# Kernel tuning notes

Measured on AMD Instinct MI355X. Metric: run time of the kernel, lower is better.

Reference implementation:

```python
import jax, jax.numpy as jnp
import numpy as np

L, S, N, E, H = 1024, 2048, 4, 512, 8
HD = E // H
LN_EPS = 1e-5


def embed_rotary(x, cos, sin):
    # x, cos, sin: (N, T, E). Rotates interleaved even/odd feature pairs.
    x2 = jnp.stack([-x[..., 1::2], x[..., ::2]], axis=-1).reshape(x.shape)
    return x * cos + x2 * sin


def setup_inputs() -> dict:
    key = jax.random.key(0)
    ks = jax.random.split(key, 8)
    query = jax.random.normal(ks[0], (L, N, E), jnp.float32)
    value = jax.random.normal(ks[1], (S, N, E), jnp.float32)
    # rotary PE tables: [..., 0] = cos, [..., 1] = sin of per-position angles
    qa = jax.random.uniform(ks[2], (N, L, E), jnp.float32, 0.0, 2.0 * np.pi)
    ka = jax.random.uniform(ks[3], (N, S, E), jnp.float32, 0.0, 2.0 * np.pi)
    query_pos = jnp.stack([jnp.cos(qa), jnp.sin(qa)], axis=-1)
    value_pos = jnp.stack([jnp.cos(ka), jnp.sin(ka)], axis=-1)
    w_scale = 1.0 / np.sqrt(E)
    in_proj_weight = jax.random.normal(ks[4], (3 * E, E), jnp.float32) * w_scale
    in_proj_bias = jnp.zeros((3 * E,), jnp.float32)
    out_proj_weight = jax.random.normal(ks[5], (E, E), jnp.float32) * w_scale
    out_proj_bias = jnp.zeros((E,), jnp.float32)
    ln_gamma = jnp.ones((E,), jnp.float32)
    ln_beta = jnp.zeros((E,), jnp.float32)
    return {
        'query': query, 'value': value,
        'query_pos': query_pos, 'value_pos': value_pos,
        'in_proj_weight': in_proj_weight, 'in_proj_bias': in_proj_bias,
        'out_proj_weight': out_proj_weight, 'out_proj_bias': out_proj_bias,
        'ln_gamma': ln_gamma, 'ln_beta': ln_beta,
    }


def reference(query, value, query_pos, value_pos,
              in_proj_weight, in_proj_bias,
              out_proj_weight, out_proj_bias,
              ln_gamma, ln_beta):
    Lq, Nb, Em = query.shape
    scaling = (Em // H) ** -0.5
    # kv_same path of the custom MHA: q from W[:E], (k, v) from W[E:] chunked
    q = query @ in_proj_weight[:Em].T + in_proj_bias[:Em]
    kv = value @ in_proj_weight[Em:].T + in_proj_bias[Em:]
    k, v = kv[..., :Em], kv[..., Em:]
    q = q * scaling
    # rotary PE (applied batch-first, then back to (L, N, E))
    q = embed_rotary(q.transpose(1, 0, 2), query_pos[..., 0], query_pos[..., 1]).transpose(1, 0, 2)
    k = embed_rotary(k.transpose(1, 0, 2), value_pos[..., 0], value_pos[..., 1]).transpose(1, 0, 2)
    # (L, N, E) -> (N, H, L, HD), matching torch view(L, N*H, HD).transpose(0, 1)
    qh = q.reshape(Lq, Nb, H, HD).transpose(1, 2, 0, 3)
    kh = k.reshape(-1, Nb, H, HD).transpose(1, 2, 0, 3)
    vh = v.reshape(-1, Nb, H, HD).transpose(1, 2, 0, 3)
    attn = jax.nn.softmax(jnp.einsum('nhld,nhsd->nhls', qh, kh), axis=-1)
    out = jnp.einsum('nhls,nhsd->nhld', attn, vh)  # (N, H, L, HD)
    out = out.transpose(2, 0, 1, 3).reshape(Lq, Nb, Em)
    out = out @ out_proj_weight.T + out_proj_bias
    # residual + LayerNorm
    y = query + out
    mu = jnp.mean(y, axis=-1, keepdims=True)
    var = jnp.mean(jnp.square(y - mu), axis=-1, keepdims=True)
    y = (y - mu) / jnp.sqrt(var + LN_EPS) * ln_gamma + ln_beta
    return y
```

## Files before the change

kernel.cpp:

```cpp
#include <hip/hip_runtime.h>
#include <math.h>

#define L_  1024
#define S_  2048
#define NB  4
#define E_  512
#define H_  8
#define HD_ 64
#define SPLIT 2

constexpr float SCALING = 0.125f;
constexpr float LOG2E   = 1.44269504f;
constexpr float LNEPS   = 1e-5f;

typedef __attribute__((ext_vector_type(8))) short s16x8;
typedef __attribute__((ext_vector_type(8))) unsigned short u16x8;
typedef __attribute__((ext_vector_type(4))) float f32x4;
typedef unsigned short ushort_t;

__device__ __forceinline__ unsigned short f2bf(float f) {
    unsigned u = __builtin_bit_cast(unsigned, f);
    u += 0x7fffu + ((u >> 16) & 1u);
    return (unsigned short)(u >> 16);
}
__device__ __forceinline__ float bf2f(unsigned short h) {
    unsigned u = ((unsigned)h) << 16;
    return __builtin_bit_cast(float, u);
}
__device__ __forceinline__ unsigned packbf(float a, float b) {
    return (unsigned)f2bf(a) | ((unsigned)f2bf(b) << 16);
}

__global__ __launch_bounds__(256)
void cast4_kernel(const float* __restrict__ s0, const float* __restrict__ s1,
                  const float* __restrict__ s2, const float* __restrict__ s3,
                  ushort_t* __restrict__ d0, ushort_t* __restrict__ d1,
                  ushort_t* __restrict__ d2, ushort_t* __restrict__ d3,
                  int c0, int c1, int c2, int c3)
{
    int i = blockIdx.x * 256 + threadIdx.x;
    const float* s; ushort_t* d; int off;
    if      (i < c0) { s = s0; d = d0; off = i; }
    else if (i < c1) { s = s1; d = d1; off = i - c0; }
    else if (i < c2) { s = s2; d = d2; off = i - c1; }
    else if (i < c3) { s = s3; d = d3; off = i - c2; }
    else return;
    const float4* sp = (const float4*)(s + (size_t)off * 8);
    float4 a = sp[0], b = sp[1];
    u16x8 o;
    o[0] = f2bf(a.x); o[1] = f2bf(a.y); o[2] = f2bf(a.z); o[3] = f2bf(a.w);
    o[4] = f2bf(b.x); o[5] = f2bf(b.y); o[6] = f2bf(b.z); o[7] = f2bf(b.w);
    *(u16x8*)(d + (size_t)off * 8) = o;
}

__global__ __launch_bounds__(256)
void qkv_gemm_kernel(const ushort_t* __restrict__ qbf,
                     const ushort_t* __restrict__ vbf,
                     const ushort_t* __restrict__ wbf,
                     ushort_t* __restrict__ qC,
                     ushort_t* __restrict__ kvC)
{
    __shared__ ushort_t As[128 * 32];
    __shared__ ushort_t Bs[128 * 32];
    const int t = threadIdx.x;
    const int w = t >> 6, l = t & 63;
    const int wr = w >> 1, wc = w & 1;
    const int g = l >> 4, c16 = l & 15;

    const int bid = blockIdx.x;
    const ushort_t *A, *W;
    ushort_t* C;
    int nfeat, m0, n0;
    if (bid < 128) {
        A = qbf; W = wbf; C = qC; nfeat = 512;
        n0 = (bid & 3) * 128; m0 = (bid >> 2) * 128;
    } else {
        int b = bid - 128;
        A = vbf; W = wbf + 512 * 512; C = kvC; nfeat = 1024;
        n0 = (b & 7) * 128; m0 = (b >> 3) * 128;
    }

    f32x4 acc[4][4];
    #pragma unroll
    for (int m = 0; m < 4; ++m)
        #pragma unroll
        for (int n = 0; n < 4; ++n) acc[m][n] = (f32x4){0.f, 0.f, 0.f, 0.f};

    for (int k0 = 0; k0 < 512; k0 += 32) {
        #pragma unroll
        for (int ch = t; ch < 512; ch += 256) {
            int r = ch >> 2, c = ch & 3;
            s16x8 v = *(const s16x8*)(A + (size_t)(m0 + r) * 512 + k0 + c * 8);
            int cp = c ^ ((r >> 1) & 3);
            *(s16x8*)((char*)As + r * 64 + cp * 16) = v;
        }
        #pragma unroll
        for (int ch = t; ch < 512; ch += 256) {
            int r = ch >> 2, c = ch & 3;
            s16x8 v = *(const s16x8*)(W + (size_t)(n0 + r) * 512 + k0 + c * 8);
            int cp = c ^ ((r >> 1) & 3);
            *(s16x8*)((char*)Bs + r * 64 + cp * 16) = v;
        }
        __syncthreads();
        s16x8 fa[4], fb[4];
        #pragma unroll
        for (int m = 0; m < 4; ++m) {
            int r = wr * 64 + m * 16 + c16;
            fa[m] = *(const s16x8*)((char*)As + r * 64 + ((g ^ ((r >> 1) & 3)) * 16));
        }
        #pragma unroll
        for (int n = 0; n < 4; ++n) {
            int r = wc * 64 + n * 16 + c16;
            fb[n] = *(const s16x8*)((char*)Bs + r * 64 + ((g ^ ((r >> 1) & 3)) * 16));
        }
        #pragma unroll
        for (int m = 0; m < 4; ++m)
            #pragma unroll
            for (int n = 0; n < 4; ++n)
                acc[m][n] = __builtin_amdgcn_mfma_f32_16x16x32_bf16(fa[m], fb[n], acc[m][n], 0, 0, 0);
        __syncthreads();
    }

    #pragma unroll
    for (int m = 0; m < 4; ++m) {
        #pragma unroll
        for (int n = 0; n < 4; ++n) {
            int col = n0 + wc * 64 + n * 16 + c16;
            #pragma unroll
            for (int r = 0; r < 4; ++r) {
                int row = m0 + wr * 64 + m * 16 + g * 4 + r;
                C[(size_t)row * nfeat + col] = f2bf(acc[m][n][r]);
            }
        }
    }
}

template<int MR, int EPI>
__global__ __launch_bounds__(256)
void gemm_bf16_kernel(const ushort_t* __restrict__ A,
                      const ushort_t* __restrict__ Bw,
                      ushort_t* __restrict__ Cb,
                      const float* __restrict__ bias,
                      const float* __restrict__ resid,
                      float* __restrict__ Y,
                      int nfeat)
{
    constexpr int BM = MR * 32;
    __shared__ ushort_t As[BM * 32];
    __shared__ ushort_t Bs[128 * 32];
    const int t = threadIdx.x;
    const int w = t >> 6, l = t & 63;
    const int wr = w >> 1, wc = w & 1;
    const int g = l >> 4, c16 = l & 15;
    const int m0 = blockIdx.y * BM;
    const int n0 = blockIdx.x * 128;

    f32x4 acc[MR][4];
    #pragma unroll
    for (int m = 0; m < MR; ++m)
        #pragma unroll
        for (int n = 0; n < 4; ++n) acc[m][n] = (f32x4){0.f, 0.f, 0.f, 0.f};

    for (int k0 = 0; k0 < 512; k0 += 32) {
        #pragma unroll
        for (int ch = t; ch < BM * 4; ch += 256) {
            int r = ch >> 2, c = ch & 3;
            s16x8 v = *(const s16x8*)(A + (size_t)(m0 + r) * 512 + k0 + c * 8);
            int cp = c ^ ((r >> 1) & 3);
            *(s16x8*)((char*)As + r * 64 + cp * 16) = v;
        }
        #pragma unroll
        for (int ch = t; ch < 512; ch += 256) {
            int r = ch >> 2, c = ch & 3;
            s16x8 v = *(const s16x8*)(Bw + (size_t)(n0 + r) * 512 + k0 + c * 8);
            int cp = c ^ ((r >> 1) & 3);
            *(s16x8*)((char*)Bs + r * 64 + cp * 16) = v;
        }
        __syncthreads();
        s16x8 fa[MR], fb[4];
        #pragma unroll
        for (int m = 0; m < MR; ++m) {
            int r = wr * (MR * 16) + m * 16 + c16;
            fa[m] = *(const s16x8*)((char*)As + r * 64 + ((g ^ ((r >> 1) & 3)) * 16));
        }
        #pragma unroll
        for (int n = 0; n < 4; ++n) {
            int r = wc * 64 + n * 16 + c16;
            fb[n] = *(const s16x8*)((char*)Bs + r * 64 + ((g ^ ((r >> 1) & 3)) * 16));
        }
        #pragma unroll
        for (int m = 0; m < MR; ++m)
            #pragma unroll
            for (int n = 0; n < 4; ++n)
                acc[m][n] = __builtin_amdgcn_mfma_f32_16x16x32_bf16(fa[m], fb[n], acc[m][n], 0, 0, 0);
        __syncthreads();
    }

    #pragma unroll
    for (int m = 0; m < MR; ++m) {
        #pragma unroll
        for (int n = 0; n < 4; ++n) {
            int col = n0 + wc * 64 + n * 16 + c16;
            #pragma unroll
            for (int r = 0; r < 4; ++r) {
                int row = m0 + wr * (MR * 16) + m * 16 + g * 4 + r;
                if (EPI == 0) {
                    Cb[(size_t)row * nfeat + col] = f2bf(acc[m][n][r]);
                } else {
                    float v = acc[m][n][r] + bias[col] + resid[(size_t)row * 512 + col];
                    Y[(size_t)row * 512 + col] = v;
                }
            }
        }
    }
}

__global__ __launch_bounds__(256)
void epi_q_kernel(const ushort_t* __restrict__ Cq,
                  const float* __restrict__ bias,
                  const float* __restrict__ qpos,
                  ushort_t* __restrict__ qrot)
{
    const float sc = SCALING * LOG2E;
    int tid = blockIdx.x * 256 + threadIdx.x;
    int token = tid >> 6;
    int fo = (tid & 63) * 8;
    int lq = token >> 2, n = token & 3;
    u16x8 cv = *(const u16x8*)(Cq + (size_t)token * 512 + fo);
    const float4* bp = (const float4*)(bias + fo);
    float4 b0 = bp[0], b1 = bp[1];
    float x[8];
    x[0] = (bf2f(cv[0]) + b0.x) * sc; x[1] = (bf2f(cv[1]) + b0.y) * sc;
    x[2] = (bf2f(cv[2]) + b0.z) * sc; x[3] = (bf2f(cv[3]) + b0.w) * sc;
    x[4] = (bf2f(cv[4]) + b1.x) * sc; x[5] = (bf2f(cv[5]) + b1.y) * sc;
    x[6] = (bf2f(cv[6]) + b1.z) * sc; x[7] = (bf2f(cv[7]) + b1.w) * sc;
    const float* pp = qpos + ((size_t)(n * L_ + lq) * 512 + fo) * 2;
    u16x8 o;
    #pragma unroll
    for (int jp = 0; jp < 4; ++jp) {
        float4 p = *(const float4*)(pp + jp * 4);
        float v0 = x[2 * jp], v1 = x[2 * jp + 1];
        o[2 * jp]     = f2bf(v0 * p.x - v1 * p.y);
        o[2 * jp + 1] = f2bf(v1 * p.z + v0 * p.w);
    }
    int h = fo >> 6, hd = fo & 63;
    *(u16x8*)(qrot + ((size_t)((n * H_ + h) * L_ + lq)) * HD_ + hd) = o;
}

__global__ __launch_bounds__(256)
void epi_kv_kernel(const ushort_t* __restrict__ Ckv,
                   const float* __restrict__ bias,
                   const float* __restrict__ vpos,
                   ushort_t* __restrict__ krot,
                   ushort_t* __restrict__ vperm)
{
    int tid = blockIdx.x * 256 + threadIdx.x;
    int token = tid >> 7;
    int fo = (tid & 127) * 8;
    int s = token >> 2, n = token & 3;
    u16x8 cv = *(const u16x8*)(Ckv + (size_t)token * 1024 + fo);
    const float4* bp = (const float4*)(bias + fo);
    float4 b0 = bp[0], b1 = bp[1];
    float x[8];
    x[0] = bf2f(cv[0]) + b0.x; x[1] = bf2f(cv[1]) + b0.y;
    x[2] = bf2f(cv[2]) + b0.z; x[3] = bf2f(cv[3]) + b0.w;
    x[4] = bf2f(cv[4]) + b1.x; x[5] = bf2f(cv[5]) + b1.y;
    x[6] = bf2f(cv[6]) + b1.z; x[7] = bf2f(cv[7]) + b1.w;
    u16x8 o;
    if (fo < 512) {
        const float* pp = vpos + ((size_t)(n * S_ + s) * 512 + fo) * 2;
        #pragma unroll
        for (int jp = 0; jp < 4; ++jp) {
            float4 p = *(const float4*)(pp + jp * 4);
            float v0 = x[2 * jp], v1 = x[2 * jp + 1];
            o[2 * jp]     = f2bf(v0 * p.x - v1 * p.y);
            o[2 * jp + 1] = f2bf(v1 * p.z + v0 * p.w);
        }
        int h = fo >> 6, hd = fo & 63;
        *(u16x8*)(krot + ((size_t)((n * H_ + h) * S_ + s)) * HD_ + hd) = o;
    } else {
        #pragma unroll
        for (int j = 0; j < 8; ++j) o[j] = f2bf(x[j]);
        int f = fo - 512;
        int h = f >> 6, hd = f & 63;
        *(u16x8*)(vperm + ((size_t)((n * H_ + h) * S_ + s)) * HD_ + hd) = o;
    }
}

__global__ __launch_bounds__(256)
void vtrans_kernel(const ushort_t* __restrict__ vin,
                   ushort_t* __restrict__ vout)
{
    __shared__ ushort_t T[64][68];
    const int t  = threadIdx.x;
    const int s0 = blockIdx.x * 64;
    const int h  = blockIdx.y, n = blockIdx.z;
    const ushort_t* src = vin + (size_t)((n * H_ + h) * S_ + s0) * HD_;
    #pragma unroll
    for (int p = 0; p < 4; ++p) {
        int e = p * 1024 + t * 4;
        int row = e >> 6, col = e & 63;
        *(ushort4*)&T[row][col] = *(const ushort4*)(src + row * HD_ + col);
    }
    __syncthreads();
    ushort_t* dst = vout + (size_t)(n * H_ + h) * HD_ * S_ + s0;
    #pragma unroll
    for (int p = 0; p < 4; ++p) {
        int d  = p * 16 + (t >> 4);
        int sc = (t & 15) * 4;
        ushort4 o;
        o.x = T[sc + 0][d]; o.y = T[sc + 1][d]; o.z = T[sc + 2][d]; o.w = T[sc + 3][d];
        *(ushort4*)(dst + (size_t)d * S_ + sc) = o;
    }
}

__global__ __launch_bounds__(256)
void attn_mfma_kernel(const ushort_t* __restrict__ qg,
                      const ushort_t* __restrict__ kg,
                      const ushort_t* __restrict__ vtg,
                      float* __restrict__ pctx,
                      float2* __restrict__ pml)
{
    __shared__ __align__(16) char smem[40960];
    char* Kb0 = smem;
    char* Kb1 = smem + 8192;
    char* Vb0 = smem + 16384;
    char* Vb1 = smem + 24576;
    const int t = threadIdx.x;
    const int w = t >> 6, l = t & 63;
    char* Ps = smem + 32768 + w * 2048;
    const int g = l >> 4, c16 = l & 15;
    const int h = blockIdx.y;
    const int n = blockIdx.z / SPLIT, sp = blockIdx.z % SPLIT;
    const int qb0 = blockIdx.x * 64;
    constexpr int NT = (S_ / SPLIT) / 64;

    const char* kbase  = (const char*)(kg  + (size_t)(n * H_ + h) * S_ * HD_)
                       + (size_t)sp * (S_ / SPLIT) * 128;
    const char* vtbase = (const char*)(vtg + (size_t)(n * H_ + h) * HD_ * S_)
                       + (size_t)sp * (S_ / SPLIT) * 2;

    const int qgl = qb0 + w * 16 + c16;
    const char* qrow = (const char*)(qg + (size_t)((n * H_ + h) * L_ + qgl) * HD_);
    s16x8 qf0 = *(const s16x8*)(qrow + 16 * g);
    s16x8 qf1 = *(const s16x8*)(qrow + 64 + 16 * g);

    const int srow = t >> 3;
    const int scol = (t & 7) * 16;

    float mrun = -1e30f, lrun = 0.f;
    f32x4 oacc[4];
    #pragma unroll
    for (int s2 = 0; s2 < 4; ++s2) oacc[s2] = (f32x4){0.f, 0.f, 0.f, 0.f};

    uint4 kreg[2], vreg[2];
    #pragma unroll
    for (int c = 0; c < 2; ++c) {
        int row = c * 32 + srow;
        kreg[c] = *(const uint4*)(kbase  + (size_t)row * 128 + scol);
        vreg[c] = *(const uint4*)(vtbase + (size_t)row * (S_ * 2) + scol);
    }
    #pragma unroll
    for (int c = 0; c < 2; ++c) {
        int row = c * 32 + srow;
        int sw  = scol ^ ((row & 7) << 4);
        *(uint4*)(Kb0 + row * 128 + sw) = kreg[c];
        *(uint4*)(Vb0 + row * 128 + sw) = vreg[c];
    }
    __syncthreads();

    int cur = 0;
    for (int st = 0; st < NT; ++st) {
        if (st + 1 < NT) {
            const char* kP = kbase  + (size_t)(st + 1) * 64 * 128;
            const char* vP = vtbase + (size_t)(st + 1) * 128;
            #pragma unroll
            for (int c = 0; c < 2; ++c) {
                int row = c * 32 + srow;
                kreg[c] = *(const uint4*)(kP + (size_t)row * 128 + scol);
                vreg[c] = *(const uint4*)(vP + (size_t)row * (S_ * 2) + scol);
            }
        }
        char* K = cur ? Kb1 : Kb0;
        char* V = cur ? Vb1 : Vb0;

        f32x4 sacc[4];
        #pragma unroll
        for (int sub = 0; sub < 4; ++sub) {
            int row = sub * 16 + c16;
            int x = (row & 7) << 4;
            s16x8 kf0 = *(const s16x8*)(K + row * 128 + ((16 * g) ^ x));
            s16x8 kf1 = *(const s16x8*)(K + row * 128 + ((64 + 16 * g) ^ x));
            f32x4 z = (f32x4){0.f, 0.f, 0.f, 0.f};
            z = __builtin_amdgcn_mfma_f32_16x16x32_bf16(kf0, qf0, z, 0, 0, 0);
            z = __builtin_amdgcn_mfma_f32_16x16x32_bf16(kf1, qf1, z, 0, 0, 0);
            sacc[sub] = z;
        }

        float mloc = sacc[0][0];
        #pragma unroll
        for (int sub = 0; sub < 4; ++sub)
            #pragma unroll
            for (int r = 0; r < 4; ++r) mloc = fmaxf(mloc, sacc[sub][r]);
        mloc = fmaxf(mloc, __shfl_xor(mloc, 16, 64));
        mloc = fmaxf(mloc, __shfl_xor(mloc, 32, 64));

        if (!__all(mloc - mrun <= 8.0f)) {
            float mnew = fmaxf(mrun, mloc);
            float scl = exp2f(mrun - mnew);
            float sclr[4];
            #pragma unroll
            for (int r = 0; r < 4; ++r) sclr[r] = __shfl(scl, 4 * g + r, 16);
            #pragma unroll
            for (int s2 = 0; s2 < 4; ++s2)
                #pragma unroll
                for (int r = 0; r < 4; ++r) oacc[s2][r] *= sclr[r];
            lrun *= scl;
            mrun = mnew;
        }

        float p[4][4];
        float ps = 0.f;
        #pragma unroll
        for (int sub = 0; sub < 4; ++sub)
            #pragma unroll
            for (int r = 0; r < 4; ++r) {
                float e = exp2f(sacc[sub][r] - mrun);
                p[sub][r] = e;
                ps += e;
            }
        ps += __shfl_xor(ps, 16, 64);
        ps += __shfl_xor(ps, 32, 64);
        lrun += ps;

        #pragma unroll
        for (int sub = 0; sub < 4; ++sub) {
            uint2 pk;
            pk.x = packbf(p[sub][0], p[sub][1]);
            pk.y = packbf(p[sub][2], p[sub][3]);
            int by = (32 * sub + 8 * g) ^ ((c16 & 7) << 4);
            *(uint2*)(Ps + c16 * 128 + by) = pk;
        }

        #pragma unroll
        for (int sh = 0; sh < 2; ++sh) {
            s16x8 pf = *(const s16x8*)(Ps + c16 * 128 + ((64 * sh + 16 * g) ^ ((c16 & 7) << 4)));
            #pragma unroll
            for (int s2 = 0; s2 < 4; ++s2) {
                int row = s2 * 16 + c16;
                int x = (row & 7) << 4;
                s16x8 vf = *(const s16x8*)(V + row * 128 + ((64 * sh + 16 * g) ^ x));
                oacc[s2] = __builtin_amdgcn_mfma_f32_16x16x32_bf16(pf, vf, oacc[s2], 0, 0, 0);
            }
        }

        if (st + 1 < NT) {
            char* Kn = cur ? Kb0 : Kb1;
            char* Vn = cur ? Vb0 : Vb1;
            #pragma unroll
            for (int c = 0; c < 2; ++c) {
                int row = c * 32 + srow;
                int sw  = scol ^ ((row & 7) << 4);
                *(uint4*)(Kn + row * 128 + sw) = kreg[c];
                *(uint4*)(Vn + row * 128 + sw) = vreg[c];
            }
            __syncthreads();
            cur ^= 1;
        }
    }

    float* pc = pctx + (size_t)sp * (L_ * NB * E_);
    #pragma unroll
    for (int r = 0; r < 4; ++r) {
        int q = qb0 + w * 16 + 4 * g + r;
        #pragma unroll
        for (int s2 = 0; s2 < 4; ++s2) {
            pc[((size_t)q * NB + n) * E_ + h * HD_ + s2 * 16 + c16] = oacc[s2][r];
        }
    }
    if (g == 0) {
        pml[(((size_t)sp * NB + n) * H_ + h) * L_ + qgl] = make_float2(mrun, lrun);
    }
}

__global__ __launch_bounds__(256)
void attn_combine_kernel(const float* __restrict__ pctx,
                         const float2* __restrict__ pml,
                         ushort_t* __restrict__ ctxb)
{
    int idx = blockIdx.x * 256 + threadIdx.x;
    int h  = (idx >> 6) & 7;
    int tq = idx >> 9;
    int q = tq >> 2, n = tq & 3;
    float O0 = pctx[idx];
    float O1 = pctx[(size_t)(L_ * NB * E_) + idx];
    float2 ml0 = pml[(((size_t)0 * NB + n) * H_ + h) * L_ + q];
    float2 ml1 = pml[(((size_t)1 * NB + n) * H_ + h) * L_ + q];
    float ms = fmaxf(ml0.x, ml1.x);
    float a0 = exp2f(ml0.x - ms), a1 = exp2f(ml1.x - ms);
    float num = O0 * a0 + O1 * a1;
    float den = ml0.y * a0 + ml1.y * a1;
    ctxb[idx] = f2bf(num / den);
}

__global__ __launch_bounds__(256)
void ln_kernel(float* __restrict__ y, const float* __restrict__ gamma,
               const float* __restrict__ beta)
{
    __shared__ float red1[4], red2[4];
    const int row = blockIdx.x;
    const int t   = threadIdx.x;
    float* p = y + (size_t)row * E_;
    float x0 = p[t], x1 = p[t + 256];

    float s = x0 + x1;
    #pragma unroll
    for (int o = 32; o >= 1; o >>= 1) s += __shfl_down(s, o, 64);
    if ((t & 63) == 0) red1[t >> 6] = s;
    __syncthreads();
    const float mu = (red1[0] + red1[1] + red1[2] + red1[3]) * (1.0f / E_);

    const float d0 = x0 - mu, d1 = x1 - mu;
    float vs = d0 * d0 + d1 * d1;
    #pragma unroll
    for (int o = 32; o >= 1; o >>= 1) vs += __shfl_down(vs, o, 64);
    if ((t & 63) == 0) red2[t >> 6] = vs;
    __syncthreads();
    const float var  = (red2[0] + red2[1] + red2[2] + red2[3]) * (1.0f / E_);
    const float rstd = rsqrtf(var + LNEPS);

    p[t]       = d0 * rstd * gamma[t]       + beta[t];
    p[t + 256] = d1 * rstd * gamma[t + 256] + beta[t + 256];
}

extern "C" void kernel_launch(void* const* d_in, const int* in_sizes, int n_in,
                              void* d_out, int out_size, void* d_ws, size_t ws_size,
                              hipStream_t stream) {
    const float* query = (const float*)d_in[0];
    const float* value = (const float*)d_in[1];
    const float* qpos  = (const float*)d_in[2];
    const float* vpos  = (const float*)d_in[3];
    const float* ipw   = (const float*)d_in[4];
    const float* ipb   = (const float*)d_in[5];
    const float* opw   = (const float*)d_in[6];
    const float* opb   = (const float*)d_in[7];
    const float* gamma = (const float*)d_in[8];
    const float* beta  = (const float*)d_in[9];
    float* out = (float*)d_out;

    char* ws = (char*)d_ws;
    ushort_t* kvC   = (ushort_t*)(ws);
    ushort_t* vbf   = (ushort_t*)(ws + (16u << 20));
    ushort_t* qbf   = (ushort_t*)(ws + (24u << 20));
    ushort_t* wbf   = (ushort_t*)(ws + (28u << 20));
    ushort_t* obf   = (ushort_t*)(ws + (30u << 20));
    ushort_t* qC    = (ushort_t*)(ws + (31u << 20));
    ushort_t* qrot  = (ushort_t*)(ws + (35u << 20));
    ushort_t* krot  = (ushort_t*)(ws + (39u << 20));
    ushort_t* vperm = (ushort_t*)(ws + (47u << 20));
    ushort_t* vt    = (ushort_t*)(ws);
    ushort_t* ctxb  = (ushort_t*)(ws + (8u << 20));
    float2*   pml   = (float2*)  (ws + (12u << 20));
    float*    pctx  = (float*)   (ws + (13u << 20));

    const int c0 = 262144;
    const int c1 = c0 + 524288;
    const int c2 = c1 + 98304;
    const int c3 = c2 + 32768;
    cast4_kernel<<<3584, 256, 0, stream>>>(query, value, ipw, opw,
                                           qbf, vbf, wbf, obf, c0, c1, c2, c3);

    qkv_gemm_kernel<<<640, 256, 0, stream>>>(qbf, vbf, wbf, qC, kvC);

    epi_q_kernel<<<1024, 256, 0, stream>>>(qC, ipb, qpos, qrot);
    epi_kv_kernel<<<4096, 256, 0, stream>>>(kvC, ipb + E_, vpos, krot, vperm);

    vtrans_kernel<<<dim3(S_ / 64, H_, NB), 256, 0, stream>>>(vperm, vt);

    attn_mfma_kernel<<<dim3(L_ / 64, H_, NB * SPLIT), 256, 0, stream>>>(
        qrot, krot, vt, pctx, pml);
    attn_combine_kernel<<<(L_ * NB * E_) / 256, 256, 0, stream>>>(pctx, pml, ctxb);

    gemm_bf16_kernel<1, 1><<<dim3(512 / 128, 4096 / 32), 256, 0, stream>>>(
        ctxb, obf, nullptr, opb, query, out, 512);

    ln_kernel<<<L_ * NB, 256, 0, stream>>>(out, gamma, beta);
}
```

Before: 235.6 us.

## Use direct global-to-LDS loads with double buffering and fuse split-combine into out-proj GEMM

```diff
diff --git a/kernel.cpp b/kernel.cpp
--- a/kernel.cpp
+++ b/kernel.cpp
@@ -27,8 +27,15 @@
     unsigned u = ((unsigned)h) << 16;
     return __builtin_bit_cast(float, u);
 }
-__device__ __forceinline__ unsigned packbf(float a, float b) {
-    return (unsigned)f2bf(a) | ((unsigned)f2bf(b) << 16);
+__device__ __forceinline__ unsigned cvtpk(float lo, float hi) {
+    unsigned r;
+    asm("v_cvt_pk_bf16_f32 %0, %1, %2" : "=v"(r) : "v"(lo), "v"(hi));
+    return r;
+}
+__device__ __forceinline__ void gload16(const void* g, void* l) {
+    __builtin_amdgcn_global_load_lds(
+        (const __attribute__((address_space(1))) void*)g,
+        (__attribute__((address_space(3))) void*)l, 16, 0, 0);
 }
 
 __global__ __launch_bounds__(256)
@@ -60,8 +67,8 @@
                      ushort_t* __restrict__ qC,
                      ushort_t* __restrict__ kvC)
 {
-    __shared__ ushort_t As[128 * 32];
-    __shared__ ushort_t Bs[128 * 32];
+    __shared__ ushort_t As[2][4096];
+    __shared__ ushort_t Bs[2][4096];
     const int t = threadIdx.x;
     const int w = t >> 6, l = t & 63;
     const int wr = w >> 1, wc = w & 1;
@@ -73,12 +80,21 @@
     int nfeat, m0, n0;
     if (bid < 128) {
         A = qbf; W = wbf; C = qC; nfeat = 512;
-        n0 = (bid & 3) * 128; m0 = (bid >> 2) * 128;
+        m0 = (bid & 31) * 128; n0 = (bid >> 5) * 128;
     } else {
         int b = bid - 128;
         A = vbf; W = wbf + 512 * 512; C = kvC; nfeat = 1024;
-        n0 = (b & 7) * 128; m0 = (b >> 3) * 128;
-    }
+        m0 = (b & 63) * 128; n0 = (b >> 6) * 128;
+    }
+
+    const int ch0 = w * 64 + l;
+    const int r0  = ch0 >> 2, cs0 = (ch0 & 3) ^ ((r0 >> 1) & 3);
+    const int ch1 = 256 + ch0;
+    const int r1  = ch1 >> 2, cs1 = (ch1 & 3) ^ ((r1 >> 1) & 3);
+    const ushort_t* A0 = A + (size_t)(m0 + r0) * 512 + cs0 * 8;
+    const ushort_t* A1 = A + (size_t)(m0 + r1) * 512 + cs1 * 8;
+    const ushort_t* W0 = W + (size_t)(n0 + r0) * 512 + cs0 * 8;
+    const ushort_t* W1 = W + (size_t)(n0 + r1) * 512 + cs1 * 8;
 
     f32x4 acc[4][4];
     #pragma unroll
@@ -86,39 +102,39 @@
         #pragma unroll
         for (int n = 0; n < 4; ++n) acc[m][n] = (f32x4){0.f, 0.f, 0.f, 0.f};
 
-    for (int k0 = 0; k0 < 512; k0 += 32) {
-        #pragma unroll
-        for (int ch = t; ch < 512; ch += 256) {
-            int r = ch >> 2, c = ch & 3;
-            s16x8 v = *(const s16x8*)(A + (size_t)(m0 + r) * 512 + k0 + c * 8);
-            int cp = c ^ ((r >> 1) & 3);
-            *(s16x8*)((char*)As + r * 64 + cp * 16) = v;
-        }
-        #pragma unroll
-        for (int ch = t; ch < 512; ch += 256) {
-            int r = ch >> 2, c = ch & 3;
-            s16x8 v = *(const s16x8*)(W + (size_t)(n0 + r) * 512 + k0 + c * 8);
-            int cp = c ^ ((r >> 1) & 3);
-            *(s16x8*)((char*)Bs + r * 64 + cp * 16) = v;
-        }
-        __syncthreads();
+    gload16(A0, (char*)As[0] + w * 1024);
+    gload16(A1, (char*)As[0] + 4096 + w * 1024);
+    gload16(W0, (char*)Bs[0] + w * 1024);
+    gload16(W1, (char*)Bs[0] + 4096 + w * 1024);
+    __syncthreads();
+
+    for (int kt = 0; kt < 16; ++kt) {
+        const int cur = kt & 1;
+        if (kt + 1 < 16) {
+            const int nk = (kt + 1) * 32;
+            const int nb = cur ^ 1;
+            gload16(A0 + nk, (char*)As[nb] + w * 1024);
+            gload16(A1 + nk, (char*)As[nb] + 4096 + w * 1024);
+            gload16(W0 + nk, (char*)Bs[nb] + w * 1024);
+            gload16(W1 + nk, (char*)Bs[nb] + 4096 + w * 1024);
+        }
         s16x8 fa[4], fb[4];
         #pragma unroll
         for (int m = 0; m < 4; ++m) {
             int r = wr * 64 + m * 16 + c16;
-            fa[m] = *(const s16x8*)((char*)As + r * 64 + ((g ^ ((r >> 1) & 3)) * 16));
+            fa[m] = *(const s16x8*)((char*)As[cur] + r * 64 + ((g ^ ((r >> 1) & 3)) * 16));
         }
         #pragma unroll
         for (int n = 0; n < 4; ++n) {
             int r = wc * 64 + n * 16 + c16;
-            fb[n] = *(const s16x8*)((char*)Bs + r * 64 + ((g ^ ((r >> 1) & 3)) * 16));
+            fb[n] = *(const s16x8*)((char*)Bs[cur] + r * 64 + ((g ^ ((r >> 1) & 3)) * 16));
         }
         #pragma unroll
         for (int m = 0; m < 4; ++m)
             #pragma unroll
             for (int n = 0; n < 4; ++n)
                 acc[m][n] = __builtin_amdgcn_mfma_f32_16x16x32_bf16(fa[m], fb[n], acc[m][n], 0, 0, 0);
-        __syncthreads();
+        if (kt + 1 < 16) __syncthreads();
     }
 
     #pragma unroll
@@ -130,86 +146,6 @@
             for (int r = 0; r < 4; ++r) {
                 int row = m0 + wr * 64 + m * 16 + g * 4 + r;
                 C[(size_t)row * nfeat + col] = f2bf(acc[m][n][r]);
-            }
-        }
-    }
-}
-
-template<int MR, int EPI>
-__global__ __launch_bounds__(256)
-void gemm_bf16_kernel(const ushort_t* __restrict__ A,
-                      const ushort_t* __restrict__ Bw,
-                      ushort_t* __restrict__ Cb,
-                      const float* __restrict__ bias,
-                      const float* __restrict__ resid,
-                      float* __restrict__ Y,
-                      int nfeat)
-{
-    constexpr int BM = MR * 32;
-    __shared__ ushort_t As[BM * 32];
-    __shared__ ushort_t Bs[128 * 32];
-    const int t = threadIdx.x;
-    const int w = t >> 6, l = t & 63;
-    const int wr = w >> 1, wc = w & 1;
-    const int g = l >> 4, c16 = l & 15;
-    const int m0 = blockIdx.y * BM;
-    const int n0 = blockIdx.x * 128;
-
-    f32x4 acc[MR][4];
-    #pragma unroll
-    for (int m = 0; m < MR; ++m)
-        #pragma unroll
-        for (int n = 0; n < 4; ++n) acc[m][n] = (f32x4){0.f, 0.f, 0.f, 0.f};
-
-    for (int k0 = 0; k0 < 512; k0 += 32) {
-        #pragma unroll
-        for (int ch = t; ch < BM * 4; ch += 256) {
-            int r = ch >> 2, c = ch & 3;
-            s16x8 v = *(const s16x8*)(A + (size_t)(m0 + r) * 512 + k0 + c * 8);
-            int cp = c ^ ((r >> 1) & 3);
-            *(s16x8*)((char*)As + r * 64 + cp * 16) = v;
-        }
-        #pragma unroll
-        for (int ch = t; ch < 512; ch += 256) {
-            int r = ch >> 2, c = ch & 3;
-            s16x8 v = *(const s16x8*)(Bw + (size_t)(n0 + r) * 512 + k0 + c * 8);
-            int cp = c ^ ((r >> 1) & 3);
-            *(s16x8*)((char*)Bs + r * 64 + cp * 16) = v;
-        }
-        __syncthreads();
-        s16x8 fa[MR], fb[4];
-        #pragma unroll
-        for (int m = 0; m < MR; ++m) {
-            int r = wr * (MR * 16) + m * 16 + c16;
-            fa[m] = *(const s16x8*)((char*)As + r * 64 + ((g ^ ((r >> 1) & 3)) * 16));
-        }
-        #pragma unroll
-        for (int n = 0; n < 4; ++n) {
-            int r = wc * 64 + n * 16 + c16;
-            fb[n] = *(const s16x8*)((char*)Bs + r * 64 + ((g ^ ((r >> 1) & 3)) * 16));
-        }
-        #pragma unroll
-        for (int m = 0; m < MR; ++m)
-            #pragma unroll
-            for (int n = 0; n < 4; ++n)
-                acc[m][n] = __builtin_amdgcn_mfma_f32_16x16x32_bf16(fa[m], fb[n], acc[m][n], 0, 0, 0);
-        __syncthreads();
-    }
-
-    #pragma unroll
-    for (int m = 0; m < MR; ++m) {
-        #pragma unroll
-        for (int n = 0; n < 4; ++n) {
-            int col = n0 + wc * 64 + n * 16 + c16;
-            #pragma unroll
-            for (int r = 0; r < 4; ++r) {
-                int row = m0 + wr * (MR * 16) + m * 16 + g * 4 + r;
-                if (EPI == 0) {
-                    Cb[(size_t)row * nfeat + col] = f2bf(acc[m][n][r]);
-                } else {
-                    float v = acc[m][n][r] + bias[col] + resid[(size_t)row * 512 + col];
-                    Y[(size_t)row * 512 + col] = v;
-                }
             }
         }
     }
@@ -345,41 +281,37 @@
     s16x8 qf0 = *(const s16x8*)(qrow + 16 * g);
     s16x8 qf1 = *(const s16x8*)(qrow + 64 + 16 * g);
 
-    const int srow = t >> 3;
-    const int scol = (t & 7) * 16;
+    const int chA = w * 64 + l;
+    const int rowA = chA >> 3, srcA = ((chA & 7) * 16) ^ ((rowA & 7) << 4);
+    const int chB = 256 + chA;
+    const int rowB = chB >> 3, srcB = ((chB & 7) * 16) ^ ((rowB & 7) << 4);
+    const char* kA = kbase + (size_t)rowA * 128 + srcA;
+    const char* kB = kbase + (size_t)rowB * 128 + srcB;
+    const char* vA = vtbase + (size_t)rowA * (S_ * 2) + srcA;
+    const char* vB = vtbase + (size_t)rowB * (S_ * 2) + srcB;
 
     float mrun = -1e30f, lrun = 0.f;
     f32x4 oacc[4];
     #pragma unroll
     for (int s2 = 0; s2 < 4; ++s2) oacc[s2] = (f32x4){0.f, 0.f, 0.f, 0.f};
 
-    uint4 kreg[2], vreg[2];
-    #pragma unroll
-    for (int c = 0; c < 2; ++c) {
-        int row = c * 32 + srow;
-        kreg[c] = *(const uint4*)(kbase  + (size_t)row * 128 + scol);
-        vreg[c] = *(const uint4*)(vtbase + (size_t)row * (S_ * 2) + scol);
-    }
-    #pragma unroll
-    for (int c = 0; c < 2; ++c) {
-        int row = c * 32 + srow;
-        int sw  = scol ^ ((row & 7) << 4);
-        *(uint4*)(Kb0 + row * 128 + sw) = kreg[c];
-        *(uint4*)(Vb0 + row * 128 + sw) = vreg[c];
-    }
+    gload16(kA, Kb0 + w * 1024);
+    gload16(kB, Kb0 + 4096 + w * 1024);
+    gload16(vA, Vb0 + w * 1024);
+    gload16(vB, Vb0 + 4096 + w * 1024);
     __syncthreads();
 
     int cur = 0;
     for (int st = 0; st < NT; ++st) {
         if (st + 1 < NT) {
-            const char* kP = kbase  + (size_t)(st + 1) * 64 * 128;
-            const char* vP = vtbase + (size_t)(st + 1) * 128;
-            #pragma unroll
-            for (int c = 0; c < 2; ++c) {
-                int row = c * 32 + srow;
-                kreg[c] = *(const uint4*)(kP + (size_t)row * 128 + scol);
-                vreg[c] = *(const uint4*)(vP + (size_t)row * (S_ * 2) + scol);
-            }
+            const size_t ko = (size_t)(st + 1) * 64 * 128;
+            const size_t vo = (size_t)(st + 1) * 128;
+            char* Kn = cur ? Kb0 : Kb1;
+            char* Vn = cur ? Vb0 : Vb1;
+            gload16(kA + ko, Kn + w * 1024);
+            gload16(kB + ko, Kn + 4096 + w * 1024);
+            gload16(vA + vo, Vn + w * 1024);
+            gload16(vB + vo, Vn + 4096 + w * 1024);
         }
         char* K = cur ? Kb1 : Kb0;
         char* V = cur ? Vb1 : Vb0;
@@ -436,8 +368,8 @@
         #pragma unroll
         for (int sub = 0; sub < 4; ++sub) {
             uint2 pk;
-            pk.x = packbf(p[sub][0], p[sub][1]);
-            pk.y = packbf(p[sub][2], p[sub][3]);
+            pk.x = cvtpk(p[sub][0], p[sub][1]);
+            pk.y = cvtpk(p[sub][2], p[sub][3]);
             int by = (32 * sub + 8 * g) ^ ((c16 & 7) << 4);
             *(uint2*)(Ps + c16 * 128 + by) = pk;
         }
@@ -455,15 +387,6 @@
         }
 
         if (st + 1 < NT) {
-            char* Kn = cur ? Kb0 : Kb1;
-            char* Vn = cur ? Vb0 : Vb1;
-            #pragma unroll
-            for (int c = 0; c < 2; ++c) {
-                int row = c * 32 + srow;
-                int sw  = scol ^ ((row & 7) << 4);
-                *(uint4*)(Kn + row * 128 + sw) = kreg[c];
-                *(uint4*)(Vn + row * 128 + sw) = vreg[c];
-            }
             __syncthreads();
             cur ^= 1;
         }
@@ -484,23 +407,104 @@
 }
 
 __global__ __launch_bounds__(256)
-void attn_combine_kernel(const float* __restrict__ pctx,
-                         const float2* __restrict__ pml,
-                         ushort_t* __restrict__ ctxb)
-{
-    int idx = blockIdx.x * 256 + threadIdx.x;
-    int h  = (idx >> 6) & 7;
-    int tq = idx >> 9;
-    int q = tq >> 2, n = tq & 3;
-    float O0 = pctx[idx];
-    float O1 = pctx[(size_t)(L_ * NB * E_) + idx];
-    float2 ml0 = pml[(((size_t)0 * NB + n) * H_ + h) * L_ + q];
-    float2 ml1 = pml[(((size_t)1 * NB + n) * H_ + h) * L_ + q];
-    float ms = fmaxf(ml0.x, ml1.x);
-    float a0 = exp2f(ml0.x - ms), a1 = exp2f(ml1.x - ms);
-    float num = O0 * a0 + O1 * a1;
-    float den = ml0.y * a0 + ml1.y * a1;
-    ctxb[idx] = f2bf(num / den);
+void out_gemm_kernel(const float* __restrict__ pctx,
+                     const float2* __restrict__ pml,
+                     const ushort_t* __restrict__ Bw,
+                     const float* __restrict__ bias,
+                     const float* __restrict__ resid,
+                     float* __restrict__ Y)
+{
+    __shared__ ushort_t As[2][1024];
+    __shared__ ushort_t Bs[2][4096];
+    const int t = threadIdx.x;
+    const int w = t >> 6, l = t & 63;
+    const int wr = w >> 1, wc = w & 1;
+    const int g = l >> 4, c16 = l & 15;
+    const int m0 = blockIdx.x * 32;
+    const int n0 = blockIdx.y * 128;
+
+    const int ch0 = w * 64 + l;
+    const int rB0 = ch0 >> 2, cB0 = (ch0 & 3) ^ ((rB0 >> 1) & 3);
+    const int ch1 = 256 + ch0;
+    const int rB1 = ch1 >> 2, cB1 = (ch1 & 3) ^ ((rB1 >> 1) & 3);
+    const ushort_t* W0 = Bw + (size_t)(n0 + rB0) * 512 + cB0 * 8;
+    const ushort_t* W1 = Bw + (size_t)(n0 + rB1) * 512 + cB1 * 8;
+
+    const int ar = t >> 2, ac = t & 3;
+    const int arow = m0 + ar;
+    const int aq = arow >> 2, an = arow & 3;
+    const int acp = ac ^ ((ar >> 1) & 3);
+
+    f32x4 acc[4];
+    #pragma unroll
+    for (int n = 0; n < 4; ++n) acc[n] = (f32x4){0.f, 0.f, 0.f, 0.f};
+
+    auto stageA = [&](int buf, int k0) {
+        if (t < 128) {
+            int e0 = k0 + ac * 8;
+            int hh = e0 >> 6;
+            float2 ml0 = pml[(((size_t)0 * NB + an) * H_ + hh) * L_ + aq];
+            float2 ml1 = pml[(((size_t)1 * NB + an) * H_ + hh) * L_ + aq];
+            float ms = fmaxf(ml0.x, ml1.x);
+            float a0 = exp2f(ml0.x - ms), a1 = exp2f(ml1.x - ms);
+            float rd = 1.0f / (ml0.y * a0 + ml1.y * a1);
+            float w0 = a0 * rd, w1 = a1 * rd;
+            const float* p0 = pctx + (size_t)arow * 512 + e0;
+            const float* p1 = p0 + (size_t)L_ * NB * E_;
+            float4 x0 = *(const float4*)p0, x1 = *(const float4*)(p0 + 4);
+            float4 y0 = *(const float4*)p1, y1 = *(const float4*)(p1 + 4);
+            u16x8 o;
+            o[0] = f2bf(x0.x * w0 + y0.x * w1);
+            o[1] = f2bf(x0.y * w0 + y0.y * w1);
+            o[2] = f2bf(x0.z * w0 + y0.z * w1);
+            o[3] = f2bf(x0.w * w0 + y0.w * w1);
+            o[4] = f2bf(x1.x * w0 + y1.x * w1);
+            o[5] = f2bf(x1.y * w0 + y1.y * w1);
+            o[6] = f2bf(x1.z * w0 + y1.z * w1);
+            o[7] = f2bf(x1.w * w0 + y1.w * w1);
+            *(u16x8*)((char*)As[buf] + ar * 64 + acp * 16) = o;
+        }
+    };
+
+    stageA(0, 0);
+    gload16(W0, (char*)Bs[0] + w * 1024);
+    gload16(W1, (char*)Bs[0] + 4096 + w * 1024);
+    __syncthreads();
+
+    for (int kt = 0; kt < 16; ++kt) {
+        const int cur = kt & 1;
+        if (kt + 1 < 16) {
+            const int nk = (kt + 1) * 32;
+            const int nb = cur ^ 1;
+            stageA(nb, nk);
+            gload16(W0 + nk, (char*)Bs[nb] + w * 1024);
+            gload16(W1 + nk, (char*)Bs[nb] + 4096 + w * 1024);
+        }
+        s16x8 fa, fb[4];
+        {
+            int r = wr * 16 + c16;
+            fa = *(const s16x8*)((char*)As[cur] + r * 64 + ((g ^ ((r >> 1) & 3)) * 16));
+        }
+        #pragma unroll
+        for (int n = 0; n < 4; ++n) {
+            int r = wc * 64 + n * 16 + c16;
+            fb[n] = *(const s16x8*)((char*)Bs[cur] + r * 64 + ((g ^ ((r >> 1) & 3)) * 16));
+        }
+        #pragma unroll
+        for (int n = 0; n < 4; ++n)
+            acc[n] = __builtin_amdgcn_mfma_f32_16x16x32_bf16(fa, fb[n], acc[n], 0, 0, 0);
+        if (kt + 1 < 16) __syncthreads();
+    }
+
+    #pragma unroll
+    for (int n = 0; n < 4; ++n) {
+        int col = n0 + wc * 64 + n * 16 + c16;
+        #pragma unroll
+        for (int r = 0; r < 4; ++r) {
+            int row = m0 + wr * 16 + g * 4 + r;
+            Y[(size_t)row * 512 + col] = acc[n][r] + bias[col] + resid[(size_t)row * 512 + col];
+        }
+    }
 }
 
 __global__ __launch_bounds__(256)
@@ -559,7 +563,6 @@
     ushort_t* krot  = (ushort_t*)(ws + (39u << 20));
     ushort_t* vperm = (ushort_t*)(ws + (47u << 20));
     ushort_t* vt    = (ushort_t*)(ws);
-    ushort_t* ctxb  = (ushort_t*)(ws + (8u << 20));
     float2*   pml   = (float2*)  (ws + (12u << 20));
     float*    pctx  = (float*)   (ws + (13u << 20));
 
@@ -579,10 +582,9 @@
 
     attn_mfma_kernel<<<dim3(L_ / 64, H_, NB * SPLIT), 256, 0, stream>>>(
         qrot, krot, vt, pctx, pml);
-    attn_combine_kernel<<<(L_ * NB * E_) / 256, 256, 0, stream>>>(pctx, pml, ctxb);
-
-    gemm_bf16_kernel<1, 1><<<dim3(512 / 128, 4096 / 32), 256, 0, stream>>>(
-        ctxb, obf, nullptr, opb, query, out, 512);
+
+    out_gemm_kernel<<<dim3(128, 4), 256, 0, stream>>>(
+        pctx, pml, obf, opb, query, out);
 
     ln_kernel<<<L_ * NB, 256, 0, stream>>>(out, gamma, beta);
 }
```

After: 216.5 us. 8.1% less time.
